# Kernel tuning notes

Measured on AMD Instinct MI355X. Metric: run time of the kernel, lower is better.

Reference implementation:

```python
import jax, jax.numpy as jnp
import numpy as np

H_IN, W_IN = 128, 128  # sensor grid; region=(1,1), stride=(1,1) -> one RF per pixel


def setup_inputs() -> dict:
    key = jax.random.key(0)
    k1, k2, k3, k4, k5, k6 = jax.random.split(key, 6)
    B, N, C, HID = 8, 2048, 16, 128
    s = 1.0 / np.sqrt(HID)
    features = jax.random.normal(k1, (B, N, C), dtype=jnp.float32)
    coords = jax.random.randint(k2, (B, N, 2), 0, 128, dtype=jnp.int32)  # (x, y)
    w_ih = jax.random.normal(k3, (4 * HID, C), dtype=jnp.float32) * s
    w_hh = jax.random.normal(k4, (4 * HID, HID), dtype=jnp.float32) * s
    b_ih = jax.random.normal(k5, (4 * HID,), dtype=jnp.float32) * s
    b_hh = jax.random.normal(k6, (4 * HID,), dtype=jnp.float32) * s
    return {"features": features, "coords": coords, "w_ih": w_ih,
            "w_hh": w_hh, "b_ih": b_ih, "b_hh": b_hh}


def reference(features, coords, w_ih, w_hh, b_ih, b_hh):
    """MatrixLSTM with 1x1 non-overlapping receptive fields.

    Events (time-ordered along axis 1) are routed to their pixel's RF; a shared
    LSTM is run over each RF's event sequence and the last output per RF is
    scattered into a dense [B, hidden, H, W] map (zeros where no events).
    Implemented as one lax.scan over events with per-RF (h, c) state.
    """
    B, N, C = features.shape
    HID = w_hh.shape[1]
    # coord2idx: raster order y * W + x  -> RF id per event, [B, N]
    rf = coords[:, :, 1].astype(jnp.int32) * W_IN + coords[:, :, 0].astype(jnp.int32)
    bidx = jnp.arange(B)
    bias = b_ih + b_hh

    def step(carry, inp):
        h_all, c_all = carry              # [B, num_rf, HID] each
        x_t, rf_t = inp                   # [B, C], [B]
        h_prev = h_all[bidx, rf_t]        # gather per-RF state, [B, HID]
        c_prev = c_all[bidx, rf_t]
        gates = x_t @ w_ih.T + h_prev @ w_hh.T + bias  # [B, 4*HID]
        i, f, g, o = jnp.split(gates, 4, axis=-1)       # torch LSTM gate order
        i = jax.nn.sigmoid(i)
        f = jax.nn.sigmoid(f)
        g = jnp.tanh(g)
        o = jax.nn.sigmoid(o)
        c_new = f * c_prev + i * g
        h_new = o * jnp.tanh(c_new)
        h_all = h_all.at[bidx, rf_t].set(h_new)        # scatter back
        c_all = c_all.at[bidx, rf_t].set(c_new)
        return (h_all, c_all), None

    h0 = jnp.zeros((B, H_IN * W_IN, HID), features.dtype)
    c0 = jnp.zeros_like(h0)
    (h_all, _), _ = jax.lax.scan(step, (h0, c0),
                                 (features.transpose(1, 0, 2), rf.T))
    # final h per RF == LSTM output at each RF's last event; zeros if no events
    return h_all.reshape(B, H_IN, W_IN, HID).transpose(0, 3, 1, 2)
```

## Files before the change

### kernel.cpp

```cpp
#include <hip/hip_runtime.h>
#include <hip/hip_bf16.h>
#include <math.h>

#define B 8
#define N 2048
#define C 16
#define HID 128
#define NRF 16384
#define MAXLEN 8
#define MAXCH 2048

__device__ __forceinline__ float sigf(float x) { return 1.f / (1.f + expf(-x)); }

__global__ __launch_bounds__(256) void k_setup(
    const float* __restrict__ w_ih, const float* __restrict__ w_hh,
    const float* __restrict__ b_ih, const float* __restrict__ b_hh,
    float* __restrict__ w_ih_T, float* __restrict__ w_hh_T,
    float* __restrict__ biassum, int* __restrict__ cntrf,
    int* __restrict__ map, int* __restrict__ cnt, int* __restrict__ m2cnt) {
    int i = blockIdx.x * blockDim.x + threadIdx.x;
    cntrf[i] = 0;
    map[i] = -1;
    if (i < B) cnt[i] = 0;
    if (i < 128) m2cnt[i] = 0;
    if (i < C * 512) {
        int c = i >> 9, j = i & 511;
        w_ih_T[i] = w_ih[j * C + c];
    }
    if (i < HID * 512) {
        int k = i >> 9, j = i & 511;
        w_hh_T[i] = w_hh[j * HID + k];
    }
    if (i < 512) biassum[i] = b_ih[i] + b_hh[i];
}

__global__ __launch_bounds__(256) void k_build(
    const int* __restrict__ coords, int* __restrict__ cntrf,
    int* __restrict__ map, int* __restrict__ cnt,
    int* __restrict__ chainrf, int* __restrict__ slots) {
    int tid = threadIdx.x;
    int idx = blockIdx.x * 256 + tid;
    int b = idx >> 11;
    int n = idx & (N - 1);
    int x = coords[idx * 2 + 0];
    int y = coords[idx * 2 + 1];
    int rf = y * 128 + x;
    int pos = atomicAdd(&cntrf[b * NRF + rf], 1);
    if (pos < MAXLEN) slots[(b * NRF + rf) * MAXLEN + pos] = n;
    __shared__ int lcnt, lbase;
    if (tid == 0) lcnt = 0;
    __syncthreads();
    int r = -1;
    if (pos == 0) r = atomicAdd(&lcnt, 1);
    __syncthreads();
    if (tid == 0) lbase = atomicAdd(&cnt[b], lcnt);
    __syncthreads();
    if (pos == 0) {
        int k = lbase + r;
        chainrf[b * MAXCH + k] = rf;
        map[b * NRF + rf] = k;
    }
}

__global__ __launch_bounds__(256) void k_phase0(
    const float* __restrict__ features, const float* __restrict__ w_ih_T,
    const float* __restrict__ biassum, const int* __restrict__ cnt,
    const int* __restrict__ chainrf, const int* __restrict__ cntrf,
    int* __restrict__ slots, float* __restrict__ hfin, float* __restrict__ cfin,
    int* __restrict__ m2cnt, int* __restrict__ mlist2) {
    int tid = threadIdx.x;
    int lane = tid & 63, w = tid >> 6;
    int bb = blockIdx.x >> 5;
    __shared__ int l_idx[64], l_len[64], l_ev0[64];
    __shared__ int lm2[64];
    __shared__ int l_n, l_m2, l_b2;
    if (tid == 0) { l_n = 0; l_m2 = 0; }
    __syncthreads();
    if (tid < 64) {
        int idx = blockIdx.x * 64 + tid;
        int j = idx & (MAXCH - 1);
        if (j < cnt[bb]) {
            int bn = bb * NRF + chainrf[idx];
            int len = cntrf[bn];
            if (len > MAXLEN) len = MAXLEN;
            int* sl = slots + (size_t)bn * MAXLEN;
            int ev0;
            if (len >= 2) {
                int ev[MAXLEN];
#pragma unroll
                for (int t = 0; t < MAXLEN; t++) {
                    int v = sl[t];
                    ev[t] = (t < len) ? v : 0x7fffffff;
                }
#pragma unroll
                for (int a = 0; a < MAXLEN; a++)
#pragma unroll
                    for (int q = 0; q < MAXLEN - 1; q++) {
                        int u = ev[q], v = ev[q + 1];
                        ev[q] = min(u, v);
                        ev[q + 1] = max(u, v);
                    }
                for (int t = 0; t < len; t++) sl[t] = ev[t];
                ev0 = ev[0];
                int r2 = atomicAdd(&l_m2, 1);
                lm2[r2] = idx;
            } else {
                ev0 = sl[0];
            }
            int r = atomicAdd(&l_n, 1);
            l_idx[r] = idx; l_len[r] = len; l_ev0[r] = ev0;
        }
    }
    __syncthreads();
    if (tid == 0 && l_m2 > 0) l_b2 = atomicAdd(&m2cnt[bb * 16], l_m2);
    __syncthreads();
    if (tid < l_m2) { int p = l_b2 + tid; if (p < 256) mlist2[bb * 256 + p] = lm2[tid]; }
    int nn = l_n;
    if (nn == 0) return;
    float wi0[16], wi1[16], wg0[16], wg1[16], wo0[16], wo1[16];
#pragma unroll
    for (int c2 = 0; c2 < 16; c2++) {
        wi0[c2] = w_ih_T[c2 * 512 + lane];
        wi1[c2] = w_ih_T[c2 * 512 + lane + 64];
        wg0[c2] = w_ih_T[c2 * 512 + lane + 256];
        wg1[c2] = w_ih_T[c2 * 512 + lane + 320];
        wo0[c2] = w_ih_T[c2 * 512 + lane + 384];
        wo1[c2] = w_ih_T[c2 * 512 + lane + 448];
    }
    float bi0 = biassum[lane],       bi1 = biassum[lane + 64];
    float bg0 = biassum[lane + 256], bg1 = biassum[lane + 320];
    float bo0 = biassum[lane + 384], bo1 = biassum[lane + 448];
    for (int ii = w; ii < nn; ii += 4) {
        int idx = l_idx[ii];
        int len = l_len[ii];
        int n = l_ev0[ii];
        float f = 0.f;
        if (lane < 16) f = features[((size_t)(bb * N + n)) * C + lane];
        float ai0 = bi0, ai1 = bi1, ag0 = bg0, ag1 = bg1, ao0 = bo0, ao1 = bo1;
#pragma unroll
        for (int c2 = 0; c2 < 16; c2++) {
            float xv = __shfl(f, c2, 64);
            ai0 += wi0[c2] * xv; ai1 += wi1[c2] * xv;
            ag0 += wg0[c2] * xv; ag1 += wg1[c2] * xv;
            ao0 += wo0[c2] * xv; ao1 += wo1[c2] * xv;
        }
        float c0 = sigf(ai0) * tanhf(ag0);
        float c1 = sigf(ai1) * tanhf(ag1);
        float h0 = sigf(ao0) * tanhf(c0);
        float h1 = sigf(ao1) * tanhf(c1);
        hfin[(size_t)idx * HID + lane] = h0;
        hfin[(size_t)idx * HID + lane + 64] = h1;
        if (len >= 2) {
            cfin[(size_t)idx * HID + lane] = c0;
            cfin[(size_t)idx * HID + lane + 64] = c1;
        }
    }
}

__global__ __launch_bounds__(512) void k_recur(
    const float* __restrict__ features, const float* __restrict__ w_ih_T,
    const float* __restrict__ w_hh_T, const float* __restrict__ biassum,
    const int* __restrict__ chainrf, const int* __restrict__ cntrf,
    const int* __restrict__ slots, const int* __restrict__ m2cnt,
    const int* __restrict__ mlist2, float* __restrict__ hfin,
    const float* __restrict__ cfin) {
    int tid = threadIdx.x;
    int bb = blockIdx.x >> 7;
    int j0 = blockIdx.x & 127;
    int Mb = m2cnt[bb * 16]; if (Mb > 256) Mb = 256;
    if (j0 >= Mb) return;
    __shared__ float h_s[HID];
    __shared__ float x_s[16];
    __shared__ float g_s[512];
    float wi[16];
#pragma unroll
    for (int c2 = 0; c2 < 16; c2++) wi[c2] = w_ih_T[c2 * 512 + tid];
    float bsum = biassum[tid];
    for (int j = j0; j < Mb; j += 128) {
        int idx = mlist2[bb * 256 + j];
        int bn = bb * NRF + chainrf[idx];
        int len = cntrf[bn];
        if (len > MAXLEN) len = MAXLEN;
        const int* sl = slots + (size_t)bn * MAXLEN;
        if (tid < 128) h_s[tid] = hfin[(size_t)idx * HID + tid];
        float c = (tid < 128) ? cfin[(size_t)idx * HID + tid] : 0.f;
        __syncthreads();
        for (int t = 1; t < len; t++) {
            int n = sl[t];
            if (tid < 16) x_s[tid] = features[((size_t)(bb * N + n)) * C + tid];
            __syncthreads();
            float a0 = bsum, a1 = 0.f, a2 = 0.f, a3 = 0.f;
#pragma unroll
            for (int c2 = 0; c2 < 16; c2++) a0 += wi[c2] * x_s[c2];
#pragma unroll 8
            for (int k = 0; k < 128; k += 4) {
                a0 += w_hh_T[k * 512 + tid] * h_s[k];
                a1 += w_hh_T[(k + 1) * 512 + tid] * h_s[k + 1];
                a2 += w_hh_T[(k + 2) * 512 + tid] * h_s[k + 2];
                a3 += w_hh_T[(k + 3) * 512 + tid] * h_s[k + 3];
            }
            g_s[tid] = (a0 + a1) + (a2 + a3);
            __syncthreads();
            if (tid < 128) {
                float ig = sigf(g_s[tid]);
                float fg = sigf(g_s[tid + 128]);
                float gg = tanhf(g_s[tid + 256]);
                float og = sigf(g_s[tid + 384]);
                c = fg * c + ig * gg;
                h_s[tid] = og * tanhf(c);
            }
            __syncthreads();
        }
        if (tid < 128) hfin[(size_t)idx * HID + tid] = h_s[tid];
        __syncthreads();
    }
}

__global__ __launch_bounds__(256) void k_scatter(
    const float* __restrict__ hfin, const int* __restrict__ map,
    float* __restrict__ out) {
    int b = blockIdx.x >> 7;
    int y = blockIdx.x & 127;
    int t = threadIdx.x;
    int xq = t & 31;
    int hg = t >> 5;
    const int4* mrow = (const int4*)(map + b * NRF + y * 128);
    int4 kk = mrow[xq];
    const float* hb = hfin + (size_t)b * MAXCH * HID;
#pragma unroll
    for (int hh = 0; hh < 16; hh++) {
        int hid = hg * 16 + hh;
        float4 v;
        v.x = (kk.x < 0) ? 0.f : hb[kk.x * HID + hid];
        v.y = (kk.y < 0) ? 0.f : hb[kk.y * HID + hid];
        v.z = (kk.z < 0) ? 0.f : hb[kk.z * HID + hid];
        v.w = (kk.w < 0) ? 0.f : hb[kk.w * HID + hid];
        *(float4*)(out + ((((size_t)b * HID + hid) * 128 + y) * 128) + xq * 4) = v;
    }
}

extern "C" void kernel_launch(void* const* d_in, const int* in_sizes, int n_in,
                              void* d_out, int out_size, void* d_ws, size_t ws_size,
                              hipStream_t stream) {
    const float* features = (const float*)d_in[0];
    const int*   coords   = (const int*)d_in[1];
    const float* w_ih     = (const float*)d_in[2];
    const float* w_hh     = (const float*)d_in[3];
    const float* b_ih     = (const float*)d_in[4];
    const float* b_hh     = (const float*)d_in[5];
    float* out = (float*)d_out;

    char* ws = (char*)d_ws;
    float* w_ih_T  = (float*)(ws + 0);
    float* w_hh_T  = (float*)(ws + 32768);
    float* biassum = (float*)(ws + 294912);
    int*   cntrf   = (int*)(ws + 296960);
    int*   map     = (int*)(ws + 821248);
    int*   cnt     = (int*)(ws + 1345536);
    int*   chainrf = (int*)(ws + 1345600);
    int*   slots   = (int*)(ws + 1411136);
    float* hfin    = (float*)(ws + 5605440);
    float* cfin    = (float*)(ws + 13994048);
    int*   m2cnt   = (int*)(ws + 22382656);
    int*   mlist2  = (int*)(ws + 22383168);

    k_setup<<<dim3(B * NRF / 256), dim3(256), 0, stream>>>(
        w_ih, w_hh, b_ih, b_hh, w_ih_T, w_hh_T, biassum, cntrf, map, cnt, m2cnt);
    k_build<<<dim3(B * N / 256), dim3(256), 0, stream>>>(
        coords, cntrf, map, cnt, chainrf, slots);
    k_phase0<<<dim3(B * MAXCH / 64), dim3(256), 0, stream>>>(
        features, w_ih_T, biassum, cnt, chainrf, cntrf, slots, hfin, cfin,
        m2cnt, mlist2);
    k_recur<<<dim3(B * 128), dim3(512), 0, stream>>>(
        features, w_ih_T, w_hh_T, biassum, chainrf, cntrf, slots,
        m2cnt, mlist2, hfin, cfin);
    k_scatter<<<dim3(B * 128), dim3(256), 0, stream>>>(hfin, map, out);
}
```

Baseline: 142.5 us.

## Fuse setup and build into one per-batch LDS-histogram kernel, precompute chain lists

Merges the setup and build kernels into one launch. One 1024-thread block per batch counts events per receptive field with LDS atomics instead of global ones, which removes the global clear of the per-RF count array. The same pass emits chain lengths and the multi-event list, so phase0 no longer does that bookkeeping. Phase0 is also reshaped to 8 chains per block with input weights staged in LDS. The cost is only 8 blocks doing the per-batch build, plus 32KB of weights loaded into LDS by every one of 2048 phase0 blocks.

```diff
diff --git a/kernel.cpp b/kernel.cpp
--- a/kernel.cpp
+++ b/kernel.cpp
@@ -12,78 +12,90 @@
 
 __device__ __forceinline__ float sigf(float x) { return 1.f / (1.f + expf(-x)); }
 
-__global__ __launch_bounds__(256) void k_setup(
-    const float* __restrict__ w_ih, const float* __restrict__ w_hh,
-    const float* __restrict__ b_ih, const float* __restrict__ b_hh,
-    float* __restrict__ w_ih_T, float* __restrict__ w_hh_T,
-    float* __restrict__ biassum, int* __restrict__ cntrf,
-    int* __restrict__ map, int* __restrict__ cnt, int* __restrict__ m2cnt) {
-    int i = blockIdx.x * blockDim.x + threadIdx.x;
-    cntrf[i] = 0;
-    map[i] = -1;
-    if (i < B) cnt[i] = 0;
-    if (i < 128) m2cnt[i] = 0;
-    if (i < C * 512) {
-        int c = i >> 9, j = i & 511;
-        w_ih_T[i] = w_ih[j * C + c];
-    }
-    if (i < HID * 512) {
-        int k = i >> 9, j = i & 511;
-        w_hh_T[i] = w_hh[j * HID + k];
-    }
-    if (i < 512) biassum[i] = b_ih[i] + b_hh[i];
-}
-
-__global__ __launch_bounds__(256) void k_build(
-    const int* __restrict__ coords, int* __restrict__ cntrf,
-    int* __restrict__ map, int* __restrict__ cnt,
-    int* __restrict__ chainrf, int* __restrict__ slots) {
+__global__ __launch_bounds__(1024) void k_pre(
+    const int* __restrict__ coords, const float* __restrict__ w_ih,
+    const float* __restrict__ w_hh, const float* __restrict__ b_ih,
+    const float* __restrict__ b_hh, float* __restrict__ w_ih_T,
+    float* __restrict__ w_hh_T, float* __restrict__ biassum,
+    int* __restrict__ map, int* __restrict__ cnt, int* __restrict__ chainrf,
+    int* __restrict__ chainlen, int* __restrict__ slots,
+    int* __restrict__ m2cnt, int* __restrict__ mlist2) {
     int tid = threadIdx.x;
-    int idx = blockIdx.x * 256 + tid;
-    int b = idx >> 11;
-    int n = idx & (N - 1);
-    int x = coords[idx * 2 + 0];
-    int y = coords[idx * 2 + 1];
-    int rf = y * 128 + x;
-    int pos = atomicAdd(&cntrf[b * NRF + rf], 1);
-    if (pos < MAXLEN) slots[(b * NRF + rf) * MAXLEN + pos] = n;
-    __shared__ int lcnt, lbase;
-    if (tid == 0) lcnt = 0;
-    __syncthreads();
-    int r = -1;
-    if (pos == 0) r = atomicAdd(&lcnt, 1);
-    __syncthreads();
-    if (tid == 0) lbase = atomicAdd(&cnt[b], lcnt);
-    __syncthreads();
-    if (pos == 0) {
-        int k = lbase + r;
-        chainrf[b * MAXCH + k] = rf;
-        map[b * NRF + rf] = k;
+    if (blockIdx.x < 8) {
+        int bb = blockIdx.x;
+        __shared__ int cnt_l[NRF];
+        __shared__ int nch_l, nmul_l;
+#pragma unroll
+        for (int i = 0; i < 16; i++) cnt_l[tid + 1024 * i] = 0;
+        if (tid == 0) { nch_l = 0; nmul_l = 0; }
+#pragma unroll
+        for (int i = 0; i < 16; i++) map[bb * NRF + tid + 1024 * i] = -1;
+        __syncthreads();
+        int n0 = tid, n1 = tid + 1024;
+        int2 c0 = ((const int2*)coords)[bb * N + n0];
+        int2 c1 = ((const int2*)coords)[bb * N + n1];
+        int rf0 = c0.y * 128 + c0.x;
+        int rf1 = c1.y * 128 + c1.x;
+        int pos0 = atomicAdd(&cnt_l[rf0], 1);
+        int pos1 = atomicAdd(&cnt_l[rf1], 1);
+        if (pos0 < MAXLEN) slots[((size_t)bb * NRF + rf0) * MAXLEN + pos0] = n0;
+        if (pos1 < MAXLEN) slots[((size_t)bb * NRF + rf1) * MAXLEN + pos1] = n1;
+        __syncthreads();
+#pragma unroll
+        for (int e = 0; e < 2; e++) {
+            int rf = e ? rf1 : rf0;
+            int pos = e ? pos1 : pos0;
+            if (pos == 0) {
+                int j = atomicAdd(&nch_l, 1);
+                int len = cnt_l[rf];
+                if (len > MAXLEN) len = MAXLEN;
+                chainrf[bb * MAXCH + j] = rf;
+                chainlen[bb * MAXCH + j] = len;
+                map[bb * NRF + rf] = j;
+                if (len >= 2) {
+                    int m = atomicAdd(&nmul_l, 1);
+                    if (m < 256) mlist2[bb * 256 + m] = bb * MAXCH + j;
+                }
+            }
+        }
+        __syncthreads();
+        if (tid == 0) {
+            cnt[bb] = nch_l;
+            m2cnt[bb * 16] = (nmul_l > 256) ? 256 : nmul_l;
+        }
+    } else {
+        int i = (blockIdx.x - 8) * 1024 + tid;
+        if (i < C * 512) {
+            int c = i >> 9, j = i & 511;
+            w_ih_T[i] = w_ih[j * C + c];
+        }
+        if (i < HID * 512) {
+            int k = i >> 9, j = i & 511;
+            w_hh_T[i] = w_hh[j * HID + k];
+        }
+        if (i < 512) biassum[i] = b_ih[i] + b_hh[i];
     }
 }
 
 __global__ __launch_bounds__(256) void k_phase0(
     const float* __restrict__ features, const float* __restrict__ w_ih_T,
     const float* __restrict__ biassum, const int* __restrict__ cnt,
-    const int* __restrict__ chainrf, const int* __restrict__ cntrf,
-    int* __restrict__ slots, float* __restrict__ hfin, float* __restrict__ cfin,
-    int* __restrict__ m2cnt, int* __restrict__ mlist2) {
+    const int* __restrict__ chainrf, const int* __restrict__ chainlen,
+    int* __restrict__ slots, float* __restrict__ hfin,
+    float* __restrict__ cfin) {
     int tid = threadIdx.x;
-    int lane = tid & 63, w = tid >> 6;
-    int bb = blockIdx.x >> 5;
-    __shared__ int l_idx[64], l_len[64], l_ev0[64];
-    __shared__ int lm2[64];
-    __shared__ int l_n, l_m2, l_b2;
-    if (tid == 0) { l_n = 0; l_m2 = 0; }
-    __syncthreads();
-    if (tid < 64) {
-        int idx = blockIdx.x * 64 + tid;
-        int j = idx & (MAXCH - 1);
-        if (j < cnt[bb]) {
-            int bn = bb * NRF + chainrf[idx];
-            int len = cntrf[bn];
-            if (len > MAXLEN) len = MAXLEN;
-            int* sl = slots + (size_t)bn * MAXLEN;
+    int bb = blockIdx.x >> 8;
+    int slot0 = (blockIdx.x & 255) * 8;
+    __shared__ float ls_w[C * 512];
+    __shared__ float ls_b[512];
+    __shared__ int l_idx[8], l_len[8], l_ev0[8];
+    int nc = cnt[bb];
+    if (tid < 8) {
+        int j = slot0 + tid;
+        int idx = bb * MAXCH + j;
+        if (j < nc) {
+            int len = chainlen[idx];
+            int* sl = slots + ((size_t)bb * NRF + chainrf[idx]) * MAXLEN;
             int ev0;
             if (len >= 2) {
                 int ev[MAXLEN];
@@ -102,47 +114,40 @@
                     }
                 for (int t = 0; t < len; t++) sl[t] = ev[t];
                 ev0 = ev[0];
-                int r2 = atomicAdd(&l_m2, 1);
-                lm2[r2] = idx;
             } else {
                 ev0 = sl[0];
             }
-            int r = atomicAdd(&l_n, 1);
-            l_idx[r] = idx; l_len[r] = len; l_ev0[r] = ev0;
-        }
-    }
+            l_idx[tid] = idx; l_len[tid] = len; l_ev0[tid] = ev0;
+        } else {
+            l_idx[tid] = -1;
+        }
+    }
+    for (int i = tid; i < C * 512; i += 256) ls_w[i] = w_ih_T[i];
+    ls_b[tid] = biassum[tid];
+    ls_b[tid + 256] = biassum[tid + 256];
     __syncthreads();
-    if (tid == 0 && l_m2 > 0) l_b2 = atomicAdd(&m2cnt[bb * 16], l_m2);
-    __syncthreads();
-    if (tid < l_m2) { int p = l_b2 + tid; if (p < 256) mlist2[bb * 256 + p] = lm2[tid]; }
-    int nn = l_n;
-    if (nn == 0) return;
-    float wi0[16], wi1[16], wg0[16], wg1[16], wo0[16], wo1[16];
-#pragma unroll
-    for (int c2 = 0; c2 < 16; c2++) {
-        wi0[c2] = w_ih_T[c2 * 512 + lane];
-        wi1[c2] = w_ih_T[c2 * 512 + lane + 64];
-        wg0[c2] = w_ih_T[c2 * 512 + lane + 256];
-        wg1[c2] = w_ih_T[c2 * 512 + lane + 320];
-        wo0[c2] = w_ih_T[c2 * 512 + lane + 384];
-        wo1[c2] = w_ih_T[c2 * 512 + lane + 448];
-    }
-    float bi0 = biassum[lane],       bi1 = biassum[lane + 64];
-    float bg0 = biassum[lane + 256], bg1 = biassum[lane + 320];
-    float bo0 = biassum[lane + 384], bo1 = biassum[lane + 448];
-    for (int ii = w; ii < nn; ii += 4) {
-        int idx = l_idx[ii];
-        int len = l_len[ii];
-        int n = l_ev0[ii];
+    int w = tid >> 6, lane = tid & 63;
+#pragma unroll
+    for (int s2 = 0; s2 < 2; s2++) {
+        int s = 2 * w + s2;
+        int idx = l_idx[s];
+        if (idx < 0) continue;
+        int len = l_len[s];
+        int n = l_ev0[s];
         float f = 0.f;
         if (lane < 16) f = features[((size_t)(bb * N + n)) * C + lane];
-        float ai0 = bi0, ai1 = bi1, ag0 = bg0, ag1 = bg1, ao0 = bo0, ao1 = bo1;
+        float ai0 = ls_b[lane],       ai1 = ls_b[lane + 64];
+        float ag0 = ls_b[lane + 256], ag1 = ls_b[lane + 320];
+        float ao0 = ls_b[lane + 384], ao1 = ls_b[lane + 448];
 #pragma unroll
         for (int c2 = 0; c2 < 16; c2++) {
             float xv = __shfl(f, c2, 64);
-            ai0 += wi0[c2] * xv; ai1 += wi1[c2] * xv;
-            ag0 += wg0[c2] * xv; ag1 += wg1[c2] * xv;
-            ao0 += wo0[c2] * xv; ao1 += wo1[c2] * xv;
+            ai0 += ls_w[c2 * 512 + lane]       * xv;
+            ai1 += ls_w[c2 * 512 + lane + 64]  * xv;
+            ag0 += ls_w[c2 * 512 + lane + 256] * xv;
+            ag1 += ls_w[c2 * 512 + lane + 320] * xv;
+            ao0 += ls_w[c2 * 512 + lane + 384] * xv;
+            ao1 += ls_w[c2 * 512 + lane + 448] * xv;
         }
         float c0 = sigf(ai0) * tanhf(ag0);
         float c1 = sigf(ai1) * tanhf(ag1);
@@ -160,14 +165,14 @@
 __global__ __launch_bounds__(512) void k_recur(
     const float* __restrict__ features, const float* __restrict__ w_ih_T,
     const float* __restrict__ w_hh_T, const float* __restrict__ biassum,
-    const int* __restrict__ chainrf, const int* __restrict__ cntrf,
+    const int* __restrict__ chainrf, const int* __restrict__ chainlen,
     const int* __restrict__ slots, const int* __restrict__ m2cnt,
     const int* __restrict__ mlist2, float* __restrict__ hfin,
     const float* __restrict__ cfin) {
     int tid = threadIdx.x;
     int bb = blockIdx.x >> 7;
     int j0 = blockIdx.x & 127;
-    int Mb = m2cnt[bb * 16]; if (Mb > 256) Mb = 256;
+    int Mb = m2cnt[bb * 16];
     if (j0 >= Mb) return;
     __shared__ float h_s[HID];
     __shared__ float x_s[16];
@@ -178,10 +183,8 @@
     float bsum = biassum[tid];
     for (int j = j0; j < Mb; j += 128) {
         int idx = mlist2[bb * 256 + j];
-        int bn = bb * NRF + chainrf[idx];
-        int len = cntrf[bn];
-        if (len > MAXLEN) len = MAXLEN;
-        const int* sl = slots + (size_t)bn * MAXLEN;
+        int len = chainlen[idx];
+        const int* sl = slots + ((size_t)bb * NRF + chainrf[idx]) * MAXLEN;
         if (tid < 128) h_s[tid] = hfin[(size_t)idx * HID + tid];
         float c = (tid < 128) ? cfin[(size_t)idx * HID + tid] : 0.f;
         __syncthreads();
@@ -251,28 +254,26 @@
     float* out = (float*)d_out;
 
     char* ws = (char*)d_ws;
-    float* w_ih_T  = (float*)(ws + 0);
-    float* w_hh_T  = (float*)(ws + 32768);
-    float* biassum = (float*)(ws + 294912);
-    int*   cntrf   = (int*)(ws + 296960);
-    int*   map     = (int*)(ws + 821248);
-    int*   cnt     = (int*)(ws + 1345536);
-    int*   chainrf = (int*)(ws + 1345600);
-    int*   slots   = (int*)(ws + 1411136);
-    float* hfin    = (float*)(ws + 5605440);
-    float* cfin    = (float*)(ws + 13994048);
-    int*   m2cnt   = (int*)(ws + 22382656);
-    int*   mlist2  = (int*)(ws + 22383168);
-
-    k_setup<<<dim3(B * NRF / 256), dim3(256), 0, stream>>>(
-        w_ih, w_hh, b_ih, b_hh, w_ih_T, w_hh_T, biassum, cntrf, map, cnt, m2cnt);
-    k_build<<<dim3(B * N / 256), dim3(256), 0, stream>>>(
-        coords, cntrf, map, cnt, chainrf, slots);
-    k_phase0<<<dim3(B * MAXCH / 64), dim3(256), 0, stream>>>(
-        features, w_ih_T, biassum, cnt, chainrf, cntrf, slots, hfin, cfin,
-        m2cnt, mlist2);
+    float* w_ih_T   = (float*)(ws + 0);
+    float* w_hh_T   = (float*)(ws + 32768);
+    float* biassum  = (float*)(ws + 294912);
+    int*   map      = (int*)(ws + 296960);
+    int*   cnt      = (int*)(ws + 821248);
+    int*   chainrf  = (int*)(ws + 821312);
+    int*   chainlen = (int*)(ws + 886848);
+    int*   slots    = (int*)(ws + 952384);
+    float* hfin     = (float*)(ws + 5146688);
+    float* cfin     = (float*)(ws + 13535296);
+    int*   m2cnt    = (int*)(ws + 21923904);
+    int*   mlist2   = (int*)(ws + 21924416);
+
+    k_pre<<<dim3(81), dim3(1024), 0, stream>>>(
+        coords, w_ih, w_hh, b_ih, b_hh, w_ih_T, w_hh_T, biassum,
+        map, cnt, chainrf, chainlen, slots, m2cnt, mlist2);
+    k_phase0<<<dim3(2048), dim3(256), 0, stream>>>(
+        features, w_ih_T, biassum, cnt, chainrf, chainlen, slots, hfin, cfin);
     k_recur<<<dim3(B * 128), dim3(512), 0, stream>>>(
-        features, w_ih_T, w_hh_T, biassum, chainrf, cntrf, slots,
+        features, w_ih_T, w_hh_T, biassum, chainrf, chainlen, slots,
         m2cnt, mlist2, hfin, cfin);
     k_scatter<<<dim3(B * 128), dim3(256), 0, stream>>>(hfin, map, out);
 }
```

Result: faster. 132.9 us (-6.7%).
